# Optimization experiments

Measured on AMD Instinct MI355X. Metric: run time of the kernel, lower is better.

The kernel has to match this reference:

```python
import jax, jax.numpy as jnp
import numpy as np

B, C_IN, N, E, C_OUT = 1, 128, 50000, 800000, 128
NEG_SLOPE = 0.3


def setup_inputs() -> dict:
    key = jax.random.key(0)
    k1, k2, k3, k4, k5 = jax.random.split(key, 5)
    in_features = jax.random.normal(k1, (B, C_IN, N), dtype=jnp.float32)
    weight = jax.random.normal(k2, (C_OUT, 2 * C_IN), dtype=jnp.float32) / np.sqrt(2 * C_IN)
    bias = jax.random.normal(k3, (C_OUT,), dtype=jnp.float32) * 0.01
    reduce_index = jax.random.randint(k4, (E,), 0, N, dtype=jnp.int64)
    gather_index = jax.random.randint(k5, (E,), 0, N, dtype=jnp.int64)
    return {"in_features": in_features, "weight": weight, "bias": bias,
            "reduce_index": reduce_index, "gather_index": gather_index}


def reference(in_features, weight, bias, reduce_index, gather_index):
    n_vertices = in_features.shape[-1]
    # gather endpoint features: [B, C, E]
    vertices = in_features[..., reduce_index]
    neighbors = in_features[..., gather_index]
    # concat [x_i, x_j - x_i] -> [B, 2C, E]
    concat = jnp.concatenate([vertices, neighbors - vertices], axis=1)
    # 1x1 Conv1d == per-edge matmul: [B, O, E]
    f_e = jnp.einsum('oc,bce->boe', weight, concat) + bias[None, :, None]
    # scatter-mean over reduce_index (include_self=False: empty segments stay 0)
    f_e_efirst = jnp.moveaxis(f_e, -1, 0)                      # [E, B, O]
    sums = jax.ops.segment_sum(f_e_efirst, reduce_index, num_segments=n_vertices)  # [N,B,O]
    counts = jax.ops.segment_sum(jnp.ones((reduce_index.shape[0],), dtype=f_e.dtype),
                                 reduce_index, num_segments=n_vertices)            # [N]
    mean = sums / jnp.maximum(counts, 1.0)[:, None, None]
    out = jnp.moveaxis(mean, 0, -1)                            # [B, O, N]
    # LeakyReLU(0.3)
    return jnp.where(out >= 0, out, NEG_SLOPE * out)
```

## Files before the change

kernel.cpp:

```cpp
#include <hip/hip_runtime.h>
#include <stddef.h>

#define CCH 128
#define CAP 64

typedef unsigned int  uint;
typedef unsigned short ushort;
typedef short bf16x8 __attribute__((ext_vector_type(8)));
typedef float f32x4  __attribute__((ext_vector_type(4)));

__device__ __forceinline__ ushort f2bf(float f) {
    uint b = __float_as_uint(f);
    b += 0x7FFFu + ((b >> 16) & 1u);
    return (ushort)(b >> 16);
}
__device__ __forceinline__ float bflo(uint u) { return __uint_as_float(u << 16); }
__device__ __forceinline__ float bfhi(uint u) { return __uint_as_float(u & 0xFFFF0000u); }

__global__ void prep_zero(const float* __restrict__ w, ushort* __restrict__ wstb,
                          int* __restrict__ zero_buf, int NZ) {
    int i = blockIdx.x * 256 + threadIdx.x;
    if (i < CCH * 256) {
        int c = i & 255;
        float v = w[i];
        if (c < 128) v -= w[i + 128];
        wstb[i] = f2bf(v);
    }
    for (int n = i; n < NZ; n += gridDim.x * 256) zero_buf[n] = 0;
}

__global__ __launch_bounds__(256) void transpose_bf16(
        const float* __restrict__ x, ushort* __restrict__ xtb, int N) {
    __shared__ float tile[CCH][33];
    int n0 = blockIdx.x * 32;
    int tid = threadIdx.x;
    {
        int tx = tid & 31, r = tid >> 5;
        int n = n0 + tx;
        #pragma unroll
        for (int k = 0; k < 16; ++k) {
            int c = k * 8 + r;
            tile[c][tx] = (n < N) ? x[(size_t)c * N + n] : 0.f;
        }
    }
    __syncthreads();
    #pragma unroll
    for (int p = 0; p < 2; ++p) {
        int nn = p * 16 + (tid >> 4);
        int c8 = (tid & 15) * 8;
        if (n0 + nn < N) {
            ushort u[8];
            #pragma unroll
            for (int j = 0; j < 8; ++j) u[j] = f2bf(tile[c8 + j][nn]);
            uint4 v;
            v.x = (uint)u[0] | ((uint)u[1] << 16);
            v.y = (uint)u[2] | ((uint)u[3] << 16);
            v.z = (uint)u[4] | ((uint)u[5] << 16);
            v.w = (uint)u[6] | ((uint)u[7] << 16);
            *(uint4*)(xtb + (size_t)(n0 + nn) * CCH + c8) = v;
        }
    }
}

#define FILL_CS 4096

__global__ __launch_bounds__(256) void fill_bucket_xcd(
        const int* __restrict__ ridx, const int* __restrict__ gidx,
        int* __restrict__ counts, int* __restrict__ bucket, int E, int psz) {
    int part  = blockIdx.x & 7;
    int chunk = blockIdx.x >> 3;
    int e0 = chunk * FILL_CS;
    int e1 = e0 + FILL_CS; if (e1 > E) e1 = E;
    for (int e = e0 + threadIdx.x; e < e1; e += 256) {
        int r = ridx[e];
        int g = gidx[e];
        if (r / psz == part) {
            int p = atomicAdd(&counts[r], 1);
            if (p < CAP) bucket[r * CAP + p] = g;
        }
    }
}

__global__ __launch_bounds__(256) void gather_mean(
        const uint2* __restrict__ xtb,
        const int*   __restrict__ counts,
        const int*   __restrict__ bucket,
        ushort*      __restrict__ gmb,
        int N) {
    int wave = threadIdx.x >> 6;
    int l = threadIdx.x & 63;
    int lq = l & 31;
    int half = l >> 5;
    #pragma unroll
    for (int i = 0; i < 2; ++i) {
        int n = blockIdx.x * 8 + wave * 2 + i;
        if (n >= N) return;
        int deg = __builtin_amdgcn_readfirstlane(counts[n]);
        int dg  = (deg < CAP) ? deg : CAP;
        const int* row = bucket + n * CAP;
        float4 acc = make_float4(0.f, 0.f, 0.f, 0.f);
        int k = 0;
        for (; k + 16 <= dg; k += 16) {
            uint2 u[8];
            #pragma unroll
            for (int q = 0; q < 8; ++q) {
                int g = row[k + 2 * q + half];
                u[q] = xtb[(size_t)g * 32 + lq];
            }
            #pragma unroll
            for (int q = 0; q < 8; ++q) {
                acc.x += bflo(u[q].x); acc.y += bfhi(u[q].x);
                acc.z += bflo(u[q].y); acc.w += bfhi(u[q].y);
            }
        }
        for (; k + 8 <= dg; k += 8) {
            uint2 u[4];
            #pragma unroll
            for (int q = 0; q < 4; ++q) {
                int g = row[k + 2 * q + half];
                u[q] = xtb[(size_t)g * 32 + lq];
            }
            #pragma unroll
            for (int q = 0; q < 4; ++q) {
                acc.x += bflo(u[q].x); acc.y += bfhi(u[q].x);
                acc.z += bflo(u[q].y); acc.w += bfhi(u[q].y);
            }
        }
        for (; k + 2 <= dg; k += 2) {
            int g = row[k + half];
            uint2 u = xtb[(size_t)g * 32 + lq];
            acc.x += bflo(u.x); acc.y += bfhi(u.x);
            acc.z += bflo(u.y); acc.w += bfhi(u.y);
        }
        if (k < dg && half == 0) {
            int g = row[k];
            uint2 u = xtb[(size_t)g * 32 + lq];
            acc.x += bflo(u.x); acc.y += bfhi(u.x);
            acc.z += bflo(u.y); acc.w += bfhi(u.y);
        }
        acc.x += __shfl_xor(acc.x, 32);
        acc.y += __shfl_xor(acc.y, 32);
        acc.z += __shfl_xor(acc.z, 32);
        acc.w += __shfl_xor(acc.w, 32);
        float inv = (deg > 0) ? 1.f / (float)deg : 0.f;
        if (half == 0) {
            ushort4 r;
            r.x = f2bf(acc.x * inv);
            r.y = f2bf(acc.y * inv);
            r.z = f2bf(acc.z * inv);
            r.w = f2bf(acc.w * inv);
            *(ushort4*)(gmb + (size_t)n * CCH + lq * 4) = r;
        }
    }
}

__global__ __launch_bounds__(256) void gemm_mfma(
        const ushort* __restrict__ wstb,
        const ushort* __restrict__ xtb,
        const ushort* __restrict__ gmb,
        const int*    __restrict__ counts,
        const float*  __restrict__ bias,
        float* __restrict__ out,
        int N) {
    int t = threadIdx.x;
    int wv = t >> 6;
    int l  = t & 63;
    int l15 = l & 15;
    int lk  = l >> 4;
    int n = blockIdx.x * 64 + wv * 16 + l15;
    int nc = (n < N) ? n : (N - 1);

    f32x4 acc[8];
    #pragma unroll
    for (int mf = 0; mf < 8; ++mf) acc[mf] = (f32x4){0.f, 0.f, 0.f, 0.f};

    const ushort* brow_x = xtb + (size_t)nc * CCH + lk * 8;
    const ushort* brow_g = gmb + (size_t)nc * CCH + lk * 8;
    const ushort* arow   = wstb + (size_t)l15 * 256 + lk * 8;

    #pragma unroll
    for (int ks = 0; ks < 8; ++ks) {
        const ushort* bp = (ks < 4) ? (brow_x + ks * 32) : (brow_g + (ks - 4) * 32);
        bf16x8 b = *(const bf16x8*)bp;
        #pragma unroll
        for (int mf = 0; mf < 8; ++mf) {
            bf16x8 a = *(const bf16x8*)(arow + (size_t)mf * 16 * 256 + ks * 32);
            acc[mf] = __builtin_amdgcn_mfma_f32_16x16x32_bf16(a, b, acc[mf], 0, 0, 0);
        }
    }

    if (n < N) {
        float m = (counts[n] > 0) ? 1.f : 0.f;
        #pragma unroll
        for (int mf = 0; mf < 8; ++mf) {
            #pragma unroll
            for (int r = 0; r < 4; ++r) {
                int o = mf * 16 + lk * 4 + r;
                float v = (acc[mf][r] + bias[o]) * m;
                v = (v >= 0.f) ? v : 0.3f * v;
                out[(size_t)o * N + n] = v;
            }
        }
    }
}

extern "C" void kernel_launch(void* const* d_in, const int* in_sizes, int n_in,
                              void* d_out, int out_size, void* d_ws, size_t ws_size,
                              hipStream_t stream) {
    const float* x      = (const float*)d_in[0];
    const float* weight = (const float*)d_in[1];
    const float* bias   = (const float*)d_in[2];
    const int*   ridx   = (const int*)d_in[3];
    const int*   gidx   = (const int*)d_in[4];
    float* out = (float*)d_out;

    int N = in_sizes[0] / CCH;
    int E = in_sizes[3];

    char* ws = (char*)d_ws;
    size_t xtb_bytes = (((size_t)N * CCH * sizeof(ushort)) + 63) & ~(size_t)63;
    size_t n_bytes   = (((size_t)N * sizeof(int)) + 63) & ~(size_t)63;
    size_t bkt_bytes = (((size_t)N * CAP * sizeof(int)) + 63) & ~(size_t)63;
    size_t w_bytes   = (((size_t)CCH * 256 * sizeof(ushort)) + 63) & ~(size_t)63;

    size_t o = 0;
    ushort* xtb   = (ushort*)(ws + o); o += xtb_bytes;
    int*    counts= (int*)   (ws + o); o += n_bytes;
    int*    bucket= (int*)   (ws + o); o += bkt_bytes;
    ushort* wstb  = (ushort*)(ws + o); o += w_bytes;
    ushort* gmb   = (ushort*)(ws + o);

    int psz     = (N + 7) / 8;
    int nchunks = (E + FILL_CS - 1) / FILL_CS;

    prep_zero<<<128, 256, 0, stream>>>(weight, wstb, counts, N);

    transpose_bf16<<<(N + 31) / 32, 256, 0, stream>>>(x, xtb, N);

    fill_bucket_xcd<<<nchunks * 8, 256, 0, stream>>>(ridx, gidx, counts, bucket, E, psz);

    gather_mean<<<(N + 7) / 8, 256, 0, stream>>>(
        (const uint2*)xtb, counts, bucket, gmb, N);

    gemm_mfma<<<(N + 63) / 64, 256, 0, stream>>>(
        wstb, xtb, gmb, counts, bias, out, N);
}
```

Measured before the change: 127.3 us.

## Merge transpose and bucket fill into one interleaved launch with batched index loads

The bf16 transpose and the edge-bucketing kernel are combined into a single launch whose blocks alternate between the two roles. Because the two pieces of work are independent, they can share the GPU, and one launch boundary disappears. The fill loop also loads four edges' indices per thread before issuing any atomics, which raises memory-level parallelism. The cost is a larger block that must carry the shared-memory tile even for fill blocks, which may reduce occupancy. The interleaved order also changes the part-to-XCD mapping that the fill kernel's blockIdx&7 partitioning relied on.

```diff
diff --git a/kernel.cpp b/kernel.cpp
--- a/kernel.cpp
+++ b/kernel.cpp
@@ -3,6 +3,7 @@
 
 #define CCH 128
 #define CAP 64
+#define FILL_CS 4096
 
 typedef unsigned int  uint;
 typedef unsigned short ushort;
@@ -29,54 +30,72 @@
     for (int n = i; n < NZ; n += gridDim.x * 256) zero_buf[n] = 0;
 }
 
-__global__ __launch_bounds__(256) void transpose_bf16(
-        const float* __restrict__ x, ushort* __restrict__ xtb, int N) {
+__global__ __launch_bounds__(256) void transpose_fill(
+        const float* __restrict__ x, ushort* __restrict__ xtb,
+        const int* __restrict__ ridx, const int* __restrict__ gidx,
+        int* __restrict__ counts, int* __restrict__ bucket,
+        int N, int E, int psz, int T, int F) {
     __shared__ float tile[CCH][33];
-    int n0 = blockIdx.x * 32;
+    int b = blockIdx.x;
+    int mtf = (T < F) ? T : F;
+    int twice = 2 * mtf;
+    bool is_t; int sub;
+    if (b < twice) { is_t = !(b & 1); sub = b >> 1; }
+    else           { is_t = (T > F);  sub = (b - twice) + mtf; }
     int tid = threadIdx.x;
-    {
-        int tx = tid & 31, r = tid >> 5;
-        int n = n0 + tx;
+
+    if (is_t) {
+        int n0 = sub * 32;
+        {
+            int tx = tid & 31, r = tid >> 5;
+            int n = n0 + tx;
+            #pragma unroll
+            for (int k = 0; k < 16; ++k) {
+                int c = k * 8 + r;
+                tile[c][tx] = (n < N) ? x[(size_t)c * N + n] : 0.f;
+            }
+        }
+        __syncthreads();
         #pragma unroll
-        for (int k = 0; k < 16; ++k) {
-            int c = k * 8 + r;
-            tile[c][tx] = (n < N) ? x[(size_t)c * N + n] : 0.f;
-        }
-    }
-    __syncthreads();
-    #pragma unroll
-    for (int p = 0; p < 2; ++p) {
-        int nn = p * 16 + (tid >> 4);
-        int c8 = (tid & 15) * 8;
-        if (n0 + nn < N) {
-            ushort u[8];
-            #pragma unroll
-            for (int j = 0; j < 8; ++j) u[j] = f2bf(tile[c8 + j][nn]);
-            uint4 v;
-            v.x = (uint)u[0] | ((uint)u[1] << 16);
-            v.y = (uint)u[2] | ((uint)u[3] << 16);
-            v.z = (uint)u[4] | ((uint)u[5] << 16);
-            v.w = (uint)u[6] | ((uint)u[7] << 16);
-            *(uint4*)(xtb + (size_t)(n0 + nn) * CCH + c8) = v;
-        }
-    }
-}
-
-#define FILL_CS 4096
-
-__global__ __launch_bounds__(256) void fill_bucket_xcd(
-        const int* __restrict__ ridx, const int* __restrict__ gidx,
-        int* __restrict__ counts, int* __restrict__ bucket, int E, int psz) {
-    int part  = blockIdx.x & 7;
-    int chunk = blockIdx.x >> 3;
-    int e0 = chunk * FILL_CS;
-    int e1 = e0 + FILL_CS; if (e1 > E) e1 = E;
-    for (int e = e0 + threadIdx.x; e < e1; e += 256) {
-        int r = ridx[e];
-        int g = gidx[e];
-        if (r / psz == part) {
-            int p = atomicAdd(&counts[r], 1);
-            if (p < CAP) bucket[r * CAP + p] = g;
+        for (int p = 0; p < 2; ++p) {
+            int nn = p * 16 + (tid >> 4);
+            int c8 = (tid & 15) * 8;
+            if (n0 + nn < N) {
+                ushort u[8];
+                #pragma unroll
+                for (int j = 0; j < 8; ++j) u[j] = f2bf(tile[c8 + j][nn]);
+                uint4 v;
+                v.x = (uint)u[0] | ((uint)u[1] << 16);
+                v.y = (uint)u[2] | ((uint)u[3] << 16);
+                v.z = (uint)u[4] | ((uint)u[5] << 16);
+                v.w = (uint)u[6] | ((uint)u[7] << 16);
+                *(uint4*)(xtb + (size_t)(n0 + nn) * CCH + c8) = v;
+            }
+        }
+    } else {
+        int part  = sub & 7;
+        int chunk = sub >> 3;
+        int e0 = chunk * FILL_CS;
+        int e1 = e0 + FILL_CS; if (e1 > E) e1 = E;
+        for (int base = e0; base < e1; base += 1024) {
+            int rr[4], gg[4];
+            bool act[4];
+            #pragma unroll
+            for (int q = 0; q < 4; ++q) {
+                int e = base + q * 256 + tid;
+                bool in = (e < e1);
+                int ec = in ? e : e0;
+                rr[q] = ridx[ec];
+                gg[q] = gidx[ec];
+                act[q] = in && (rr[q] / psz == part);
+            }
+            #pragma unroll
+            for (int q = 0; q < 4; ++q) {
+                if (act[q]) {
+                    int p = atomicAdd(&counts[rr[q]], 1);
+                    if (p < CAP) bucket[rr[q] * CAP + p] = gg[q];
+                }
+            }
         }
     }
 }
@@ -232,12 +251,13 @@
 
     int psz     = (N + 7) / 8;
     int nchunks = (E + FILL_CS - 1) / FILL_CS;
+    int T = (N + 31) / 32;
+    int F = nchunks * 8;
 
     prep_zero<<<128, 256, 0, stream>>>(weight, wstb, counts, N);
 
-    transpose_bf16<<<(N + 31) / 32, 256, 0, stream>>>(x, xtb, N);
-
-    fill_bucket_xcd<<<nchunks * 8, 256, 0, stream>>>(ridx, gidx, counts, bucket, E, psz);
+    transpose_fill<<<T + F, 256, 0, stream>>>(x, xtb, ridx, gidx,
+                                              counts, bucket, N, E, psz, T, F);
 
     gather_mean<<<(N + 7) / 8, 256, 0, stream>>>(
         (const uint2*)xtb, counts, bucket, gmb, N);
```

Result: faster. 121.2 us (-4.8%).

## Pre-bin edges by destination partition before filling per-vertex buckets

Applied to the files above, without the earlier changes.

Replaces the bucket-fill kernel with two passes. Before, each of 8 partition-block groups re-read every edge and kept only its own partition's edges. The new first pass counts edges per partition with shared-memory atomics and scatters (reduce, gather) pairs into per-partition bins. The second pass then has blocks mapped to one partition fill the per-vertex buckets from that bin only. This removes the 8x redundant read of the index arrays while keeping the partition-to-block mapping, at the cost of an extra kernel launch, a bin buffer write and read, and global atomics on bin counters.

```diff
diff --git a/kernel.cpp b/kernel.cpp
--- a/kernel.cpp
+++ b/kernel.cpp
@@ -3,6 +3,8 @@
 
 #define CCH 128
 #define CAP 64
+#define NBIN 8
+#define BIN_CS 4096
 
 typedef unsigned int  uint;
 typedef unsigned short ushort;
@@ -62,21 +64,61 @@
     }
 }
 
-#define FILL_CS 4096
-
-__global__ __launch_bounds__(256) void fill_bucket_xcd(
+__global__ __launch_bounds__(256) void bin_edges(
         const int* __restrict__ ridx, const int* __restrict__ gidx,
-        int* __restrict__ counts, int* __restrict__ bucket, int E, int psz) {
-    int part  = blockIdx.x & 7;
-    int chunk = blockIdx.x >> 3;
-    int e0 = chunk * FILL_CS;
-    int e1 = e0 + FILL_CS; if (e1 > E) e1 = E;
-    for (int e = e0 + threadIdx.x; e < e1; e += 256) {
-        int r = ridx[e];
-        int g = gidx[e];
-        if (r / psz == part) {
-            int p = atomicAdd(&counts[r], 1);
-            if (p < CAP) bucket[r * CAP + p] = g;
+        int* __restrict__ bin_cnt, int2* __restrict__ binrg,
+        int E, int psz, int bcap) {
+    __shared__ int lcnt[NBIN], lbase[NBIN], lcur[NBIN];
+    int e0 = blockIdx.x * BIN_CS;
+    int tid = threadIdx.x;
+    if (tid < NBIN) lcnt[tid] = 0;
+    __syncthreads();
+    int rr[16], gg[16], pp[16];
+    #pragma unroll
+    for (int q = 0; q < 16; ++q) {
+        int e = e0 + q * 256 + tid;
+        bool in = (e < E);
+        rr[q] = in ? ridx[e] : 0;
+        gg[q] = in ? gidx[e] : 0;
+        pp[q] = in ? (rr[q] / psz) : -1;
+        if (pp[q] >= 0) atomicAdd(&lcnt[pp[q]], 1);
+    }
+    __syncthreads();
+    if (tid < NBIN) { lbase[tid] = atomicAdd(&bin_cnt[tid], lcnt[tid]); lcur[tid] = 0; }
+    __syncthreads();
+    #pragma unroll
+    for (int q = 0; q < 16; ++q) {
+        if (pp[q] >= 0) {
+            int s = atomicAdd(&lcur[pp[q]], 1);
+            int idx = lbase[pp[q]] + s;
+            if (idx < bcap)
+                binrg[(size_t)pp[q] * bcap + idx] = make_int2(rr[q], gg[q]);
+        }
+    }
+}
+
+__global__ __launch_bounds__(256) void fill_from_bins(
+        const int2* __restrict__ binrg, const int* __restrict__ bin_cnt,
+        int* __restrict__ counts, int* __restrict__ bucket, int bcap, int kb) {
+    int p   = blockIdx.x & 7;
+    int blk = blockIdx.x >> 3;
+    int cnt = bin_cnt[p];
+    if (cnt > bcap) cnt = bcap;
+    const int2* bp = binrg + (size_t)p * bcap;
+    for (int base = blk * 1024; base < cnt; base += kb * 1024) {
+        int2 u[4]; bool act[4];
+        #pragma unroll
+        for (int q = 0; q < 4; ++q) {
+            int i = base + q * 256 + threadIdx.x;
+            act[q] = (i < cnt);
+            u[q] = act[q] ? bp[i] : make_int2(0, 0);
+        }
+        #pragma unroll
+        for (int q = 0; q < 4; ++q) {
+            if (act[q]) {
+                int pos = atomicAdd(&counts[u[q].x], 1);
+                if (pos < CAP) bucket[u[q].x * CAP + pos] = u[q].y;
+            }
         }
     }
 }
@@ -217,27 +259,35 @@
     int N = in_sizes[0] / CCH;
     int E = in_sizes[3];
 
+    int psz  = (N + 7) / 8;
+    int bcap = E / NBIN + (E / 32) + 1024;
+
     char* ws = (char*)d_ws;
     size_t xtb_bytes = (((size_t)N * CCH * sizeof(ushort)) + 63) & ~(size_t)63;
     size_t n_bytes   = (((size_t)N * sizeof(int)) + 63) & ~(size_t)63;
     size_t bkt_bytes = (((size_t)N * CAP * sizeof(int)) + 63) & ~(size_t)63;
     size_t w_bytes   = (((size_t)CCH * 256 * sizeof(ushort)) + 63) & ~(size_t)63;
+    size_t bin_bytes = (((size_t)NBIN * bcap * sizeof(int2)) + 63) & ~(size_t)63;
 
     size_t o = 0;
-    ushort* xtb   = (ushort*)(ws + o); o += xtb_bytes;
-    int*    counts= (int*)   (ws + o); o += n_bytes;
-    int*    bucket= (int*)   (ws + o); o += bkt_bytes;
-    ushort* wstb  = (ushort*)(ws + o); o += w_bytes;
-    ushort* gmb   = (ushort*)(ws + o);
-
-    int psz     = (N + 7) / 8;
-    int nchunks = (E + FILL_CS - 1) / FILL_CS;
-
-    prep_zero<<<128, 256, 0, stream>>>(weight, wstb, counts, N);
+    ushort* xtb    = (ushort*)(ws + o); o += xtb_bytes;
+    int*    counts = (int*)   (ws + o); o += n_bytes;
+    int*    bin_cnt= (int*)   (ws + o); o += 64;
+    int*    bucket = (int*)   (ws + o); o += bkt_bytes;
+    ushort* wstb   = (ushort*)(ws + o); o += w_bytes;
+    ushort* gmb    = (ushort*)(ws + o); o += xtb_bytes;
+    int2*   binrg  = (int2*)  (ws + o); o += bin_bytes;
+
+    prep_zero<<<128, 256, 0, stream>>>(weight, wstb, counts, N + 16);
 
     transpose_bf16<<<(N + 31) / 32, 256, 0, stream>>>(x, xtb, N);
 
-    fill_bucket_xcd<<<nchunks * 8, 256, 0, stream>>>(ridx, gidx, counts, bucket, E, psz);
+    int bblocks = (E + BIN_CS - 1) / BIN_CS;
+    bin_edges<<<bblocks, 256, 0, stream>>>(ridx, gidx, bin_cnt, binrg, E, psz, bcap);
+
+    int kb = 128;
+    fill_from_bins<<<kb * NBIN, 256, 0, stream>>>(binrg, bin_cnt, counts, bucket,
+                                                  bcap, kb);
 
     gather_mean<<<(N + 7) / 8, 256, 0, stream>>>(
         (const uint2*)xtb, counts, bucket, gmb, N);
```

Result: slower. 137.8 us (+8.2%).
